# Optimization experiments

Hardware: AMD Instinct MI355X
Metric: run time of the kernel (lower is better)

The kernel has to match this reference:

```python
import jax, jax.numpy as jnp
import numpy as np

N = 100000   # nodes
E = 1600000  # edges per relation
R = 6        # relations
D_IN = 128
H = 64
K = 3


def setup_inputs() -> dict:
    key = jax.random.key(0)
    ks = jax.random.split(key, 20)
    def g(k, shape, scale=0.05):
        return jax.random.normal(k, shape, dtype=jnp.float32) * scale
    return {
        "x": jax.random.normal(ks[0], (N, D_IN), dtype=jnp.float32),
        "edge_index": jax.random.randint(ks[1], (R, 2, E), 0, N, dtype=jnp.int32),
        "cheb1_w": g(ks[2], (R, K, D_IN, H)),
        "cheb1_b": g(ks[3], (R, H)),
        "cheb2_w": g(ks[4], (R, K, H, H)),
        "cheb2_b": g(ks[5], (R, H)),
        "gate_w1": g(ks[6], (H, H)),
        "gate_b1": g(ks[7], (H,)),
        "gate_w2": g(ks[8], (H, 1)),
        "gate_b2": g(ks[9], (1,)),
        "proj_w": g(ks[10], (H, H)),
        "proj_b": g(ks[11], (H,)),
        "cls_w1": g(ks[12], (H, H)),
        "cls_b1": g(ks[13], (H,)),
        "cls_w2": g(ks[14], (H, 1)),
        "cls_b2": g(ks[15], (1,)),
        "aux_w": g(ks[16], (R, H)),
        "aux_b": g(ks[17], (R,)),
    }


def cheb_conv(x, src, dst, W, b, n):
    """PyG ChebConv, sym normalization, lambda_max=2 => L_hat = -D^{-1/2} A D^{-1/2}.
    W: [K, in, out]. Messages flow src -> dst (scatter-add at dst)."""
    deg = jax.ops.segment_sum(jnp.ones(src.shape, x.dtype), src, num_segments=n)
    dis = jnp.where(deg > 0, 1.0 / jnp.sqrt(jnp.maximum(deg, 1e-12)), 0.0)
    norm = -(dis[src] * dis[dst])  # [E]
    def lhat(v):  # sparse SpMM: [N, F] -> [N, F]
        return jax.ops.segment_sum(norm[:, None] * v[src], dst, num_segments=n)
    tx0 = x
    out = tx0 @ W[0]
    tx1 = lhat(x)
    out = out + tx1 @ W[1]
    for k in range(2, W.shape[0]):
        tx2 = 2.0 * lhat(tx1) - tx0
        out = out + tx2 @ W[k]
        tx0, tx1 = tx1, tx2
    return out + b


def reference(x, edge_index, cheb1_w, cheb1_b, cheb2_w, cheb2_b,
              gate_w1, gate_b1, gate_w2, gate_b2, proj_w, proj_b,
              cls_w1, cls_b1, cls_w2, cls_b2, aux_w, aux_b):
    n = x.shape[0]
    hs = []
    for r in range(edge_index.shape[0]):  # small fixed relation set
        src, dst = edge_index[r, 0], edge_index[r, 1]
        h = jax.nn.relu(cheb_conv(x, src, dst, cheb1_w[r], cheb1_b[r], n))
        h = jax.nn.relu(cheb_conv(h, src, dst, cheb2_w[r], cheb2_b[r], n))
        hs.append(h)
    stack = jnp.stack(hs, axis=1)  # [N, R, H]
    # RelationGate: per-(node, relation) MLP -> softmax over relations
    gate_logits = jax.nn.relu(stack @ gate_w1 + gate_b1) @ gate_w2 + gate_b2  # [N, R, 1]
    alpha = jax.nn.softmax(gate_logits, axis=1)
    h_fused = jnp.sum(alpha * stack, axis=1)  # [N, H]
    h_proj = jax.nn.relu(h_fused @ proj_w + proj_b)
    logit = (jax.nn.relu(h_proj @ cls_w1 + cls_b1) @ cls_w2 + cls_b2)[:, 0]  # [N]
    aux = jnp.einsum('nrh,rh->nr', stack, aux_w) + aux_b  # [N, R] aux logits per relation
    return logit, aux
```

## Files before the change

### kernel.cpp

```cpp
#include <hip/hip_runtime.h>
#include <hip/hip_bf16.h>

#define NN 100000
#define EE 1600000
#define RR 6
#define NBK 391
#define EB 391
#define CAP 4608

typedef __attribute__((ext_vector_type(8))) short bf16x8;
typedef __attribute__((ext_vector_type(4))) float f32x4;

__device__ inline short f2b(float x) {
    __hip_bfloat16 h = __float2bfloat16(x);
    return *reinterpret_cast<short*>(&h);
}
__device__ inline float b2f(short s) {
    __hip_bfloat16 h = *reinterpret_cast<__hip_bfloat16*>(&s);
    return __bfloat162float(h);
}


__global__ __launch_bounds__(256) void zero_cnts(int* p, int n) {
    int i = blockIdx.x * 256 + threadIdx.x;
    if (i < n) p[i] = 0;
}

__global__ __launch_bounds__(256) void bin_scatter(const int* __restrict__ src,
                                                   const int* __restrict__ dst,
                                                   int* __restrict__ bcurD,
                                                   int* __restrict__ bcurS,
                                                   unsigned* __restrict__ pairs,
                                                   unsigned char* __restrict__ srcs) {
    __shared__ int lcD[NBK], lbD[NBK], loD[NBK];
    __shared__ int lcS[NBK], lbS[NBK], loS[NBK];
    int t = threadIdx.x;
    for (int i = t; i < NBK; i += 256) { lcD[i] = 0; loD[i] = 0; lcS[i] = 0; loS[i] = 0; }
    __syncthreads();
    int base = blockIdx.x * 4096;
#pragma unroll
    for (int i = 0; i < 16; ++i) {
        int e = base + i * 256 + t;
        if (e < EE) {
            atomicAdd(&lcD[dst[e] >> 8], 1);
            atomicAdd(&lcS[src[e] >> 8], 1);
        }
    }
    __syncthreads();
    for (int i = t; i < NBK; i += 256) {
        lbD[i] = lcD[i] ? atomicAdd(&bcurD[i], lcD[i]) : 0;
        lbS[i] = lcS[i] ? atomicAdd(&bcurS[i], lcS[i]) : 0;
    }
    __syncthreads();
#pragma unroll
    for (int i = 0; i < 16; ++i) {
        int e = base + i * 256 + t;
        if (e < EE) {
            int s = src[e], d = dst[e];
            int bD = d >> 8, bS = s >> 8;
            int pD = lbD[bD] + atomicAdd(&loD[bD], 1);
            if (pD >= 0 && pD < CAP)
                pairs[(size_t)bD * CAP + pD] = ((unsigned)s << 8) | (unsigned)(d & 255);
            int pS = lbS[bS] + atomicAdd(&loS[bS], 1);
            if (pS >= 0 && pS < CAP)
                srcs[(size_t)bS * CAP + pS] = (unsigned char)(s & 255);
        }
    }
}

__global__ __launch_bounds__(512) void csr_build(const unsigned* __restrict__ pairs,
                                                 const int* __restrict__ bcurD,
                                                 int* __restrict__ rowp2,
                                                 int* __restrict__ csr) {
    __shared__ int hist[2048];
    __shared__ int wsums[4];
    int b = blockIdx.x, t = threadIdx.x;
    int p0 = b * CAP;
    int cnt = min(bcurD[b], CAP);
    int p1 = p0 + cnt;
    for (int i = t; i < 2048; i += 512) hist[i] = 0;
    __syncthreads();
    for (int e = p0 + t; e < p1; e += 512) {
        unsigned pr = pairs[e];
        int key = ((pr & 255) << 3) | (int)((pr >> 8) >> 14);
        atomicAdd(&hist[key], 1);
    }
    __syncthreads();
    int s[8] = {0, 0, 0, 0, 0, 0, 0, 0};
    int run = 0, x = 0;
    int lane = t & 63, wv = t >> 6;
    if (t < 256) {
#pragma unroll
        for (int i = 0; i < 8; ++i) { s[i] = run; run += hist[t * 8 + i]; }
        x = run;
#pragma unroll
        for (int d = 1; d < 64; d <<= 1) {
            int y = __shfl_up(x, d, 64);
            if (lane >= d) x += y;
        }
        if (lane == 63) wsums[wv] = x;
    }
    __syncthreads();
    if (t < 256) {
        int woff = 0;
        for (int wi = 0; wi < wv; ++wi) woff += wsums[wi];
        int excl = woff + x - run;
        rowp2[b * 257 + t] = p0 + excl;
        if (t == 0) rowp2[b * 257 + 256] = p1;
#pragma unroll
        for (int i = 0; i < 8; ++i) hist[t * 8 + i] = p0 + excl + s[i];
    }
    __syncthreads();
    for (int e = p0 + t; e < p1; e += 512) {
        unsigned pr = pairs[e];
        int key = ((pr & 255) << 3) | (int)((pr >> 8) >> 14);
        int pos = atomicAdd(&hist[key], 1);
        if (pos >= 0 && pos < NBK * CAP) csr[pos] = (int)(pr >> 8);
    }
}

__global__ __launch_bounds__(256) void deg_dis(const unsigned char* __restrict__ srcs,
                                               const int* __restrict__ bcurS,
                                               float* __restrict__ dis) {
    __shared__ int hist[256];
    int b = blockIdx.x, t = threadIdx.x;
    hist[t] = 0;
    __syncthreads();
    int cnt = min(bcurS[b], CAP);
    const unsigned char* sp = srcs + (size_t)b * CAP;
    for (int e = t; e < cnt; e += 256)
        atomicAdd(&hist[sp[e]], 1);
    __syncthreads();
    int node = b * 256 + t;
    if (node < NN) {
        int d = hist[t];
        dis[node] = d > 0 ? rsqrtf((float)d) : 0.f;
    }
}

__global__ __launch_bounds__(256) void cvt_x(const float* __restrict__ x, short* __restrict__ xb) {
    int i = blockIdx.x * 256 + threadIdx.x;
    if (i >= NN * 128 / 8) return;
    const float* p = x + (size_t)i * 8;
    float4 u0 = *(const float4*)p;
    float4 u1 = *(const float4*)(p + 4);
    bf16x8 t;
    t[0] = f2b(u0.x); t[1] = f2b(u0.y); t[2] = f2b(u0.z); t[3] = f2b(u0.w);
    t[4] = f2b(u1.x); t[5] = f2b(u1.y); t[6] = f2b(u1.z); t[7] = f2b(u1.w);
    *(bf16x8*)(xb + (size_t)i * 8) = t;
}

__global__ __launch_bounds__(256) void wpack_cheb(const float* __restrict__ W, int Kin, int KS,
                                                  short* __restrict__ bh, short* __restrict__ bl) {
    int idx = blockIdx.x * 256 + threadIdx.x;
    int l = idx & 63;
    int q = idx >> 6;
    int s = q % KS; q /= KS;
    int t = q % 12; q /= 12;
    int r = q;
    if (r >= RR) return;
#pragma unroll
    for (int j = 0; j < 8; ++j) {
        int k = s * 32 + ((l >> 4) * 8) + j;
        int n = t * 16 + (l & 15);
        int g = n >> 6, jj = n & 63;
        float v = W[(((size_t)r * 3 + (g == 0 ? 0 : g)) * Kin + k) * 64 + jj];
        if (g == 0) v -= W[(((size_t)r * 3 + 2) * Kin + k) * 64 + jj];
        short hi = f2b(v);
        short lo = f2b(v - b2f(hi));
        bh[(size_t)idx * 8 + j] = hi;
        bl[(size_t)idx * 8 + j] = lo;
    }
}

__global__ __launch_bounds__(256) void wpack64(const float* __restrict__ W,
                                               short* __restrict__ bh, short* __restrict__ bl) {
    int idx = blockIdx.x * 256 + threadIdx.x;
    if (idx >= 512) return;
    int l = idx & 63;
    int s = (idx >> 6) & 1;
    int t = idx >> 7;
#pragma unroll
    for (int j = 0; j < 8; ++j) {
        int k = s * 32 + ((l >> 4) * 8) + j;
        int n = t * 16 + (l & 15);
        float v = W[k * 64 + n];
        short hi = f2b(v);
        short lo = f2b(v - b2f(hi));
        bh[(size_t)idx * 8 + j] = hi;
        bl[(size_t)idx * 8 + j] = lo;
    }
}

template <int KDIM>
__global__ __launch_bounds__(256) void gemm_mfma(const short* __restrict__ A, int lda,
                                                 const short* __restrict__ bph,
                                                 const short* __restrict__ bplo,
                                                 int nt0, int ntn, int s1, int s2,
                                                 short* __restrict__ o0, int ld0,
                                                 short* __restrict__ o1, int ld1,
                                                 short* __restrict__ o2, int ld2,
                                                 const float* __restrict__ bias,
                                                 int scale_from,
                                                 const float* __restrict__ rowscale,
                                                 int do_relu) {
    constexpr int KS = KDIM / 32;
    int w = threadIdx.x >> 6, l = threadIdx.x & 63;
    int rows0 = blockIdx.x * 64 + w * 16;
    int arow = rows0 + (l & 15);
    int kbase = (l >> 4) * 8;
    bf16x8 af[KS];
#pragma unroll
    for (int s = 0; s < KS; ++s) {
        bf16x8 t = {0, 0, 0, 0, 0, 0, 0, 0};
        if (arow < NN) t = *(const bf16x8*)(A + (size_t)arow * lda + s * 32 + kbase);
        af[s] = t;
    }
    for (int t = 0; t < ntn; ++t) {
        f32x4 acc = {0.f, 0.f, 0.f, 0.f};
        const short* bp0 = bph + (((size_t)(nt0 + t) * KS) * 64 + l) * 8;
        const short* bl0 = bplo + (((size_t)(nt0 + t) * KS) * 64 + l) * 8;
#pragma unroll
        for (int s = 0; s < KS; ++s) {
            bf16x8 bh = *(const bf16x8*)(bp0 + (size_t)s * 64 * 8);
            bf16x8 bl = *(const bf16x8*)(bl0 + (size_t)s * 64 * 8);
            acc = __builtin_amdgcn_mfma_f32_16x16x32_bf16(af[s], bh, acc, 0, 0, 0);
            acc = __builtin_amdgcn_mfma_f32_16x16x32_bf16(af[s], bl, acc, 0, 0, 0);
        }
        short* o;
        int ldc, tl;
        if (t < s1) { o = o0; ldc = ld0; tl = t; }
        else if (t < s2) { o = o1; ldc = ld1; tl = t - s1; }
        else { o = o2; ldc = ld2; tl = t - s2; }
        int lcol = (tl << 4) + (l & 15);
        bool scl = (rowscale != nullptr) && (t >= scale_from);
#pragma unroll
        for (int r_ = 0; r_ < 4; ++r_) {
            int row = rows0 + (l >> 4) * 4 + r_;
            if (row >= NN) continue;
            float v = acc[r_];
            if (bias) v += bias[lcol];
            if (do_relu) v = fmaxf(v, 0.f);
            if (scl) v *= rowscale[row];
            o[(size_t)row * ldc + lcol] = f2b(v);
        }
    }
}

template <int MID>
__global__ __launch_bounds__(256) void spmm_bf(const short* __restrict__ v,
                                               const short* __restrict__ aux,
                                               short* __restrict__ outb, int ldc,
                                               const int* __restrict__ csr,
                                               const int* __restrict__ rowp2,
                                               const float* __restrict__ dis,
                                               const float* __restrict__ bias) {
    int t = threadIdx.x;
    int wv = t >> 6, l = t & 63;
    int g = l >> 4, fl = l & 15;
    int row = blockIdx.x * 16 + wv * 4 + g;
    int b = row >> 8, ri = row & 255;
    int s0 = rowp2[b * 257 + ri];
    int s1 = rowp2[b * 257 + ri + 1];
    s0 = max(s0, b * CAP);
    s1 = min(s1, b * CAP + CAP);
    float a0 = 0.f, a1 = 0.f, a2 = 0.f, a3 = 0.f;
    int e = s0;
    int idx[8], nidx[8];
    bool have = (e + 8 <= s1);
    if (have) {
#pragma unroll
        for (int i = 0; i < 8; ++i) idx[i] = csr[e + i];
    }
    while (have) {
        uint2 u[8];
#pragma unroll
        for (int i = 0; i < 8; ++i)
            u[i] = *(const uint2*)(v + (size_t)idx[i] * 64 + fl * 4);
        int en = e + 8;
        bool nhave = (en + 8 <= s1);
        if (nhave) {
#pragma unroll
            for (int i = 0; i < 8; ++i) nidx[i] = csr[en + i];
        }
#pragma unroll
        for (int i = 0; i < 8; ++i) {
            a0 += __uint_as_float(u[i].x << 16);
            a1 += __uint_as_float(u[i].x & 0xffff0000u);
            a2 += __uint_as_float(u[i].y << 16);
            a3 += __uint_as_float(u[i].y & 0xffff0000u);
        }
#pragma unroll
        for (int i = 0; i < 8; ++i) idx[i] = nidx[i];
        e = en;
        have = nhave;
    }
    for (; e < s1; ++e) {
        uint2 u = *(const uint2*)(v + (size_t)csr[e] * 64 + fl * 4);
        a0 += __uint_as_float(u.x << 16);
        a1 += __uint_as_float(u.x & 0xffff0000u);
        a2 += __uint_as_float(u.y << 16);
        a3 += __uint_as_float(u.y & 0xffff0000u);
    }
    float d = dis[row];
    uint2 au = *(const uint2*)(aux + (size_t)row * 64 + fl * 4);
    float v0, v1, v2, v3;
    if (MID) {
        float mm = -2.f * d * d;
        v0 = __uint_as_float(au.x << 16) + mm * a0;
        v1 = __uint_as_float(au.x & 0xffff0000u) + mm * a1;
        v2 = __uint_as_float(au.y << 16) + mm * a2;
        v3 = __uint_as_float(au.y & 0xffff0000u) + mm * a3;
    } else {
        float4 bs = *(const float4*)(bias + fl * 4);
        v0 = fmaxf(__uint_as_float(au.x << 16) - d * a0 + bs.x, 0.f);
        v1 = fmaxf(__uint_as_float(au.x & 0xffff0000u) - d * a1 + bs.y, 0.f);
        v2 = fmaxf(__uint_as_float(au.y << 16) - d * a2 + bs.z, 0.f);
        v3 = fmaxf(__uint_as_float(au.y & 0xffff0000u) - d * a3 + bs.w, 0.f);
    }
    uint2 o;
    o.x = (unsigned)(unsigned short)f2b(v0) | ((unsigned)(unsigned short)f2b(v1) << 16);
    o.y = (unsigned)(unsigned short)f2b(v2) | ((unsigned)(unsigned short)f2b(v3) << 16);
    *(uint2*)(outb + (size_t)row * ldc + fl * 4) = o;
}

__global__ __launch_bounds__(256) void gate_mfma(const short* __restrict__ stack,
                                                 const short* __restrict__ g1h,
                                                 const short* __restrict__ g1l,
                                                 const float* __restrict__ gb1,
                                                 const float* __restrict__ gw2,
                                                 const float* __restrict__ gb2,
                                                 const float* __restrict__ auxw,
                                                 const float* __restrict__ auxb,
                                                 float* __restrict__ glogit,
                                                 float* __restrict__ out) {
    int w = threadIdx.x >> 6, l = threadIdx.x & 63;
    int rows0 = blockIdx.x * 64 + w * 16;
    int arow = rows0 + (l & 15);
    int kbase = (l >> 4) * 8;
    bf16x8 af[2];
#pragma unroll
    for (int s = 0; s < 2; ++s)
        af[s] = *(const bf16x8*)(stack + (size_t)arow * 64 + s * 32 + kbase);
    int rmod = arow % RR;
    float paux = 0.f;
#pragma unroll
    for (int s = 0; s < 2; ++s) {
        const float* aw = auxw + rmod * 64 + s * 32 + kbase;
#pragma unroll
        for (int j = 0; j < 8; ++j) paux = fmaf(b2f(af[s][j]), aw[j], paux);
    }
    paux += __shfl_xor(paux, 16, 64);
    paux += __shfl_xor(paux, 32, 64);
    if (l < 16) out[NN + (size_t)rows0 + l] = paux + auxb[rmod];
    float p[4] = {0.f, 0.f, 0.f, 0.f};
#pragma unroll
    for (int t = 0; t < 4; ++t) {
        f32x4 acc = {0.f, 0.f, 0.f, 0.f};
#pragma unroll
        for (int s = 0; s < 2; ++s) {
            bf16x8 bh = *(const bf16x8*)(g1h + (((size_t)t * 2 + s) * 64 + l) * 8);
            bf16x8 bl = *(const bf16x8*)(g1l + (((size_t)t * 2 + s) * 64 + l) * 8);
            acc = __builtin_amdgcn_mfma_f32_16x16x32_bf16(af[s], bh, acc, 0, 0, 0);
            acc = __builtin_amdgcn_mfma_f32_16x16x32_bf16(af[s], bl, acc, 0, 0, 0);
        }
        int col = t * 16 + (l & 15);
        float b = gb1[col], w2 = gw2[col];
#pragma unroll
        for (int r_ = 0; r_ < 4; ++r_) {
            float h = fmaxf(acc[r_] + b, 0.f);
            p[r_] = fmaf(h, w2, p[r_]);
        }
    }
#pragma unroll
    for (int d = 1; d < 16; d <<= 1) {
#pragma unroll
        for (int r_ = 0; r_ < 4; ++r_) p[r_] += __shfl_xor(p[r_], d, 64);
    }
    if ((l & 15) == 0) {
        float g2 = gb2[0];
#pragma unroll
        for (int r_ = 0; r_ < 4; ++r_) glogit[rows0 + (l >> 4) * 4 + r_] = p[r_] + g2;
    }
}

__global__ __launch_bounds__(256) void fuse_kernel(const short* __restrict__ stack,
                                                   const float* __restrict__ glogit,
                                                   short* __restrict__ hfused) {
    int tid = threadIdx.x;
    int w = tid >> 6, lane = tid & 63;
    int n = blockIdx.x * 4 + w;
    if (n >= NN) return;
    float gl[RR];
    float m = -1e30f;
#pragma unroll
    for (int r = 0; r < RR; r++) {
        gl[r] = glogit[(size_t)n * RR + r];
        m = fmaxf(m, gl[r]);
    }
    float ssum = 0.f;
#pragma unroll
    for (int r = 0; r < RR; r++) {
        gl[r] = __expf(gl[r] - m);
        ssum += gl[r];
    }
    float inv = 1.f / ssum;
    float hf = 0.f;
#pragma unroll
    for (int r = 0; r < RR; r++) {
        float s = b2f(stack[((size_t)n * RR + r) * 64 + lane]);
        hf = fmaf(gl[r] * inv, s, hf);
    }
    hfused[(size_t)n * 64 + lane] = f2b(hf);
}

__global__ __launch_bounds__(256) void cls_mfma(const short* __restrict__ hproj,
                                                const short* __restrict__ c1h,
                                                const short* __restrict__ c1l,
                                                const float* __restrict__ cb1,
                                                const float* __restrict__ cw2,
                                                const float* __restrict__ cb2,
                                                float* __restrict__ out) {
    int w = threadIdx.x >> 6, l = threadIdx.x & 63;
    int rows0 = blockIdx.x * 64 + w * 16;
    int arow = rows0 + (l & 15);
    int kbase = (l >> 4) * 8;
    bf16x8 af[2];
#pragma unroll
    for (int s = 0; s < 2; ++s) {
        bf16x8 t = {0, 0, 0, 0, 0, 0, 0, 0};
        if (arow < NN) t = *(const bf16x8*)(hproj + (size_t)arow * 64 + s * 32 + kbase);
        af[s] = t;
    }
    float p[4] = {0.f, 0.f, 0.f, 0.f};
#pragma unroll
    for (int t = 0; t < 4; ++t) {
        f32x4 acc = {0.f, 0.f, 0.f, 0.f};
#pragma unroll
        for (int s = 0; s < 2; ++s) {
            bf16x8 bh = *(const bf16x8*)(c1h + (((size_t)t * 2 + s) * 64 + l) * 8);
            bf16x8 bl = *(const bf16x8*)(c1l + (((size_t)t * 2 + s) * 64 + l) * 8);
            acc = __builtin_amdgcn_mfma_f32_16x16x32_bf16(af[s], bh, acc, 0, 0, 0);
            acc = __builtin_amdgcn_mfma_f32_16x16x32_bf16(af[s], bl, acc, 0, 0, 0);
        }
        int col = t * 16 + (l & 15);
        float b = cb1[col], w2 = cw2[col];
#pragma unroll
        for (int r_ = 0; r_ < 4; ++r_) {
            float h = fmaxf(acc[r_] + b, 0.f);
            p[r_] = fmaf(h, w2, p[r_]);
        }
    }
#pragma unroll
    for (int d = 1; d < 16; d <<= 1) {
#pragma unroll
        for (int r_ = 0; r_ < 4; ++r_) p[r_] += __shfl_xor(p[r_], d, 64);
    }
    if ((l & 15) == 0) {
        float c2 = cb2[0];
#pragma unroll
        for (int r_ = 0; r_ < 4; ++r_) {
            int row = rows0 + (l >> 4) * 4 + r_;
            if (row < NN) out[row] = p[r_] + c2;
        }
    }
}


extern "C" void kernel_launch(void* const* d_in, const int* in_sizes, int n_in,
                              void* d_out, int out_size, void* d_ws, size_t ws_size,
                              hipStream_t stream) {
    const float* x = (const float*)d_in[0];
    const int* ei = (const int*)d_in[1];
    const float* c1w = (const float*)d_in[2];
    const float* c1b = (const float*)d_in[3];
    const float* c2w = (const float*)d_in[4];
    const float* c2b = (const float*)d_in[5];
    const float* gw1 = (const float*)d_in[6];
    const float* gb1 = (const float*)d_in[7];
    const float* gw2 = (const float*)d_in[8];
    const float* gb2 = (const float*)d_in[9];
    const float* pw = (const float*)d_in[10];
    const float* pb = (const float*)d_in[11];
    const float* cw1 = (const float*)d_in[12];
    const float* cb1 = (const float*)d_in[13];
    const float* cw2 = (const float*)d_in[14];
    const float* cb2 = (const float*)d_in[15];
    const float* auxw = (const float*)d_in[16];
    const float* auxb = (const float*)d_in[17];
    float* out = (float*)d_out;

    char* wsp = (char*)d_ws;
    size_t off = 0;
    auto carve = [&](size_t bytes) -> char* {
        char* p = wsp + off;
        off += (bytes + 255) & ~(size_t)255;
        return p;
    };
    short* stack = (short*)carve((size_t)NN * RR * 64 * 2);
    short* y1b = (short*)carve((size_t)NN * 64 * 2);
    short* y2b = (short*)carve((size_t)NN * 64 * 2);
    short* wb = (short*)carve((size_t)NN * 64 * 2);
    short* h1 = (short*)carve((size_t)NN * 64 * 2);
    short* t0b = (short*)carve((size_t)NN * 64 * 2);
    short* xb = (short*)carve((size_t)NN * 128 * 2);
    float* dis = (float*)carve((size_t)NN * 4);
    int* rowp2 = (int*)carve((size_t)NBK * 257 * 4);
    int* csr = (int*)carve((size_t)NBK * CAP * 4);
    int* cnts = (int*)carve((size_t)2 * RR * NBK * 4);
    short* bp1h = (short*)carve((size_t)RR * 12 * 4 * 64 * 8 * 2);
    short* bp1l = (short*)carve((size_t)RR * 12 * 4 * 64 * 8 * 2);
    short* bp2h = (short*)carve((size_t)RR * 12 * 2 * 64 * 8 * 2);
    short* bp2l = (short*)carve((size_t)RR * 12 * 2 * 64 * 8 * 2);
    short* g1h = (short*)carve((size_t)512 * 8 * 2);
    short* g1l = (short*)carve((size_t)512 * 8 * 2);
    short* pwh = (short*)carve((size_t)512 * 8 * 2);
    short* pwl = (short*)carve((size_t)512 * 8 * 2);
    short* c1h = (short*)carve((size_t)512 * 8 * 2);
    short* c1l = (short*)carve((size_t)512 * 8 * 2);
    float* glogit = (float*)carve((size_t)NN * RR * 4);
    unsigned* pairs = (unsigned*)y1b;
    unsigned char* srcs = (unsigned char*)y2b;
    short* hfused = h1;
    short* hproj = y2b;
    (void)in_sizes; (void)n_in; (void)out_size;

    if (off > ws_size) return;

    zero_cnts<<<(2 * RR * NBK + 255) / 256, 256, 0, stream>>>(cnts, 2 * RR * NBK);
    cvt_x<<<(NN * 128 / 8 + 255) / 256, 256, 0, stream>>>(x, xb);
    wpack_cheb<<<72, 256, 0, stream>>>(c1w, 128, 4, bp1h, bp1l);
    wpack_cheb<<<36, 256, 0, stream>>>(c2w, 64, 2, bp2h, bp2l);
    wpack64<<<2, 256, 0, stream>>>(gw1, g1h, g1l);
    wpack64<<<2, 256, 0, stream>>>(pw, pwh, pwl);
    wpack64<<<2, 256, 0, stream>>>(cw1, c1h, c1l);

    const int GB = 1563;
    for (int r = 0; r < RR; ++r) {
        const int* src = ei + (size_t)r * 2 * EE;
        const int* dst = src + EE;
        const short* b1h = bp1h + (size_t)r * 12 * 4 * 64 * 8;
        const short* b1l = bp1l + (size_t)r * 12 * 4 * 64 * 8;
        const short* b2h = bp2h + (size_t)r * 12 * 2 * 64 * 8;
        const short* b2l = bp2l + (size_t)r * 12 * 2 * 64 * 8;
        int* bcurD = cnts + (size_t)(2 * r + 0) * NBK;
        int* bcurS = cnts + (size_t)(2 * r + 1) * NBK;

        bin_scatter<<<EB, 256, 0, stream>>>(src, dst, bcurD, bcurS, pairs, srcs);
        csr_build<<<NBK, 512, 0, stream>>>(pairs, bcurD, rowp2, csr);
        deg_dis<<<NBK, 256, 0, stream>>>(srcs, bcurS, dis);

        gemm_mfma<128><<<GB, 256, 0, stream>>>(xb, 128, b1h, b1l, 0, 12, 4, 8,
                                               t0b, 64, y1b, 64, y2b, 64,
                                               nullptr, 4, dis, 0);
        spmm_bf<1><<<NN / 16, 256, 0, stream>>>(y2b, y1b, wb, 64, csr, rowp2, dis, nullptr);
        spmm_bf<0><<<NN / 16, 256, 0, stream>>>(wb, t0b, h1, 64, csr, rowp2, dis,
                                                c1b + r * 64);
        gemm_mfma<64><<<GB, 256, 0, stream>>>(h1, 64, b2h, b2l, 0, 12, 4, 8,
                                              t0b, 64, y1b, 64, y2b, 64,
                                              nullptr, 4, dis, 0);
        spmm_bf<1><<<NN / 16, 256, 0, stream>>>(y2b, y1b, wb, 64, csr, rowp2, dis, nullptr);
        spmm_bf<0><<<NN / 16, 256, 0, stream>>>(wb, t0b, stack + r * 64, RR * 64,
                                                csr, rowp2, dis, c2b + r * 64);
    }
    gate_mfma<<<9375, 256, 0, stream>>>(stack, g1h, g1l, gb1, gw2, gb2,
                                        auxw, auxb, glogit, out);
    fuse_kernel<<<NN / 4, 256, 0, stream>>>(stack, glogit, hfused);
    gemm_mfma<64><<<GB, 256, 0, stream>>>(hfused, 64, pwh, pwl, 0, 4, 4, 8,
                                          hproj, 64, nullptr, 0, nullptr, 0,
                                          pb, 99, nullptr, 1);
    cls_mfma<<<GB, 256, 0, stream>>>(hproj, c1h, c1l, cb1, cw2, cb2, out);
}
```

Before: 1.711 ms.

## Widen SpMM loads, fuse gate with softmax fusion, enlarge binning blocks

Result: no change. 1.725 ms (+0.8%).

```diff
diff --git a/kernel.cpp b/kernel.cpp
--- a/kernel.cpp
+++ b/kernel.cpp
@@ -5,7 +5,7 @@
 #define EE 1600000
 #define RR 6
 #define NBK 391
-#define EB 391
+#define EB2 196
 #define CAP 4608
 
 typedef __attribute__((ext_vector_type(8))) short bf16x8;
@@ -18,6 +18,11 @@
 __device__ inline float b2f(short s) {
     __hip_bfloat16 h = *reinterpret_cast<__hip_bfloat16*>(&s);
     return __bfloat162float(h);
+}
+__device__ inline float ulo(unsigned u) { return __uint_as_float(u << 16); }
+__device__ inline float uhi(unsigned u) { return __uint_as_float(u & 0xffff0000u); }
+__device__ inline unsigned pck(float a, float b) {
+    return (unsigned)(unsigned short)f2b(a) | ((unsigned)(unsigned short)f2b(b) << 16);
 }
 
 
@@ -37,9 +42,9 @@
     int t = threadIdx.x;
     for (int i = t; i < NBK; i += 256) { lcD[i] = 0; loD[i] = 0; lcS[i] = 0; loS[i] = 0; }
     __syncthreads();
-    int base = blockIdx.x * 4096;
-#pragma unroll
-    for (int i = 0; i < 16; ++i) {
+    int base = blockIdx.x * 8192;
+#pragma unroll
+    for (int i = 0; i < 32; ++i) {
         int e = base + i * 256 + t;
         if (e < EE) {
             atomicAdd(&lcD[dst[e] >> 8], 1);
@@ -53,7 +58,7 @@
     }
     __syncthreads();
 #pragma unroll
-    for (int i = 0; i < 16; ++i) {
+    for (int i = 0; i < 32; ++i) {
         int e = base + i * 256 + t;
         if (e < EE) {
             int s = src[e], d = dst[e];
@@ -257,14 +262,15 @@
                                                const float* __restrict__ bias) {
     int t = threadIdx.x;
     int wv = t >> 6, l = t & 63;
-    int g = l >> 4, fl = l & 15;
-    int row = blockIdx.x * 16 + wv * 4 + g;
+    int g = l >> 3, fl = l & 7;
+    int row = blockIdx.x * 32 + wv * 8 + g;
+    if (row >= NN) return;
     int b = row >> 8, ri = row & 255;
     int s0 = rowp2[b * 257 + ri];
     int s1 = rowp2[b * 257 + ri + 1];
     s0 = max(s0, b * CAP);
     s1 = min(s1, b * CAP + CAP);
-    float a0 = 0.f, a1 = 0.f, a2 = 0.f, a3 = 0.f;
+    float a[8] = {0.f, 0.f, 0.f, 0.f, 0.f, 0.f, 0.f, 0.f};
     int e = s0;
     int idx[8], nidx[8];
     bool have = (e + 8 <= s1);
@@ -273,10 +279,10 @@
         for (int i = 0; i < 8; ++i) idx[i] = csr[e + i];
     }
     while (have) {
-        uint2 u[8];
+        uint4 u[8];
 #pragma unroll
         for (int i = 0; i < 8; ++i)
-            u[i] = *(const uint2*)(v + (size_t)idx[i] * 64 + fl * 4);
+            u[i] = *(const uint4*)(v + (size_t)idx[i] * 64 + fl * 8);
         int en = e + 8;
         bool nhave = (en + 8 <= s1);
         if (nhave) {
@@ -285,10 +291,10 @@
         }
 #pragma unroll
         for (int i = 0; i < 8; ++i) {
-            a0 += __uint_as_float(u[i].x << 16);
-            a1 += __uint_as_float(u[i].x & 0xffff0000u);
-            a2 += __uint_as_float(u[i].y << 16);
-            a3 += __uint_as_float(u[i].y & 0xffff0000u);
+            a[0] += ulo(u[i].x); a[1] += uhi(u[i].x);
+            a[2] += ulo(u[i].y); a[3] += uhi(u[i].y);
+            a[4] += ulo(u[i].z); a[5] += uhi(u[i].z);
+            a[6] += ulo(u[i].w); a[7] += uhi(u[i].w);
         }
 #pragma unroll
         for (int i = 0; i < 8; ++i) idx[i] = nidx[i];
@@ -296,35 +302,35 @@
         have = nhave;
     }
     for (; e < s1; ++e) {
-        uint2 u = *(const uint2*)(v + (size_t)csr[e] * 64 + fl * 4);
-        a0 += __uint_as_float(u.x << 16);
-        a1 += __uint_as_float(u.x & 0xffff0000u);
-        a2 += __uint_as_float(u.y << 16);
-        a3 += __uint_as_float(u.y & 0xffff0000u);
+        uint4 u = *(const uint4*)(v + (size_t)csr[e] * 64 + fl * 8);
+        a[0] += ulo(u.x); a[1] += uhi(u.x);
+        a[2] += ulo(u.y); a[3] += uhi(u.y);
+        a[4] += ulo(u.z); a[5] += uhi(u.z);
+        a[6] += ulo(u.w); a[7] += uhi(u.w);
     }
     float d = dis[row];
-    uint2 au = *(const uint2*)(aux + (size_t)row * 64 + fl * 4);
-    float v0, v1, v2, v3;
+    uint4 au = *(const uint4*)(aux + (size_t)row * 64 + fl * 8);
+    float av[8] = {ulo(au.x), uhi(au.x), ulo(au.y), uhi(au.y),
+                   ulo(au.z), uhi(au.z), ulo(au.w), uhi(au.w)};
+    float vv[8];
     if (MID) {
         float mm = -2.f * d * d;
-        v0 = __uint_as_float(au.x << 16) + mm * a0;
-        v1 = __uint_as_float(au.x & 0xffff0000u) + mm * a1;
-        v2 = __uint_as_float(au.y << 16) + mm * a2;
-        v3 = __uint_as_float(au.y & 0xffff0000u) + mm * a3;
+#pragma unroll
+        for (int i = 0; i < 8; ++i) vv[i] = av[i] + mm * a[i];
     } else {
-        float4 bs = *(const float4*)(bias + fl * 4);
-        v0 = fmaxf(__uint_as_float(au.x << 16) - d * a0 + bs.x, 0.f);
-        v1 = fmaxf(__uint_as_float(au.x & 0xffff0000u) - d * a1 + bs.y, 0.f);
-        v2 = fmaxf(__uint_as_float(au.y << 16) - d * a2 + bs.z, 0.f);
-        v3 = fmaxf(__uint_as_float(au.y & 0xffff0000u) - d * a3 + bs.w, 0.f);
-    }
-    uint2 o;
-    o.x = (unsigned)(unsigned short)f2b(v0) | ((unsigned)(unsigned short)f2b(v1) << 16);
-    o.y = (unsigned)(unsigned short)f2b(v2) | ((unsigned)(unsigned short)f2b(v3) << 16);
-    *(uint2*)(outb + (size_t)row * ldc + fl * 4) = o;
-}
-
-__global__ __launch_bounds__(256) void gate_mfma(const short* __restrict__ stack,
+        float4 bs0 = *(const float4*)(bias + fl * 8);
+        float4 bs1 = *(const float4*)(bias + fl * 8 + 4);
+        float bb[8] = {bs0.x, bs0.y, bs0.z, bs0.w, bs1.x, bs1.y, bs1.z, bs1.w};
+#pragma unroll
+        for (int i = 0; i < 8; ++i) vv[i] = fmaxf(av[i] - d * a[i] + bb[i], 0.f);
+    }
+    uint4 o;
+    o.x = pck(vv[0], vv[1]); o.y = pck(vv[2], vv[3]);
+    o.z = pck(vv[4], vv[5]); o.w = pck(vv[6], vv[7]);
+    *(uint4*)(outb + (size_t)row * ldc + fl * 8) = o;
+}
+
+__global__ __launch_bounds__(384) void gate_fuse(const short* __restrict__ stack,
                                                  const short* __restrict__ g1h,
                                                  const short* __restrict__ g1l,
                                                  const float* __restrict__ gb1,
@@ -332,86 +338,112 @@
                                                  const float* __restrict__ gb2,
                                                  const float* __restrict__ auxw,
                                                  const float* __restrict__ auxb,
-                                                 float* __restrict__ glogit,
+                                                 short* __restrict__ hfused,
                                                  float* __restrict__ out) {
-    int w = threadIdx.x >> 6, l = threadIdx.x & 63;
-    int rows0 = blockIdx.x * 64 + w * 16;
-    int arow = rows0 + (l & 15);
+    __shared__ float glog[384];
+    __shared__ float alpha[64][6];
+    int t = threadIdx.x;
+    int w = t / 64, l = t & 63;
+    int nb = blockIdx.x * 64;
+    int rowsw = nb * 6 + w * 64;
     int kbase = (l >> 4) * 8;
-    bf16x8 af[2];
-#pragma unroll
-    for (int s = 0; s < 2; ++s)
-        af[s] = *(const bf16x8*)(stack + (size_t)arow * 64 + s * 32 + kbase);
-    int rmod = arow % RR;
-    float paux = 0.f;
-#pragma unroll
-    for (int s = 0; s < 2; ++s) {
-        const float* aw = auxw + rmod * 64 + s * 32 + kbase;
-#pragma unroll
-        for (int j = 0; j < 8; ++j) paux = fmaf(b2f(af[s][j]), aw[j], paux);
-    }
-    paux += __shfl_xor(paux, 16, 64);
-    paux += __shfl_xor(paux, 32, 64);
-    if (l < 16) out[NN + (size_t)rows0 + l] = paux + auxb[rmod];
-    float p[4] = {0.f, 0.f, 0.f, 0.f};
-#pragma unroll
-    for (int t = 0; t < 4; ++t) {
-        f32x4 acc = {0.f, 0.f, 0.f, 0.f};
+    bf16x8 af[4][2];
+#pragma unroll
+    for (int q = 0; q < 4; ++q) {
+        int arow = rowsw + q * 16 + (l & 15);
+        bool ok = arow < NN * RR;
 #pragma unroll
         for (int s = 0; s < 2; ++s) {
-            bf16x8 bh = *(const bf16x8*)(g1h + (((size_t)t * 2 + s) * 64 + l) * 8);
-            bf16x8 bl = *(const bf16x8*)(g1l + (((size_t)t * 2 + s) * 64 + l) * 8);
-            acc = __builtin_amdgcn_mfma_f32_16x16x32_bf16(af[s], bh, acc, 0, 0, 0);
-            acc = __builtin_amdgcn_mfma_f32_16x16x32_bf16(af[s], bl, acc, 0, 0, 0);
-        }
-        int col = t * 16 + (l & 15);
-        float b = gb1[col], w2 = gw2[col];
-#pragma unroll
-        for (int r_ = 0; r_ < 4; ++r_) {
-            float h = fmaxf(acc[r_] + b, 0.f);
-            p[r_] = fmaf(h, w2, p[r_]);
-        }
-    }
-#pragma unroll
-    for (int d = 1; d < 16; d <<= 1) {
-#pragma unroll
-        for (int r_ = 0; r_ < 4; ++r_) p[r_] += __shfl_xor(p[r_], d, 64);
-    }
-    if ((l & 15) == 0) {
-        float g2 = gb2[0];
-#pragma unroll
-        for (int r_ = 0; r_ < 4; ++r_) glogit[rows0 + (l >> 4) * 4 + r_] = p[r_] + g2;
-    }
-}
-
-__global__ __launch_bounds__(256) void fuse_kernel(const short* __restrict__ stack,
-                                                   const float* __restrict__ glogit,
-                                                   short* __restrict__ hfused) {
-    int tid = threadIdx.x;
-    int w = tid >> 6, lane = tid & 63;
-    int n = blockIdx.x * 4 + w;
-    if (n >= NN) return;
-    float gl[RR];
-    float m = -1e30f;
-#pragma unroll
-    for (int r = 0; r < RR; r++) {
-        gl[r] = glogit[(size_t)n * RR + r];
-        m = fmaxf(m, gl[r]);
-    }
-    float ssum = 0.f;
-#pragma unroll
-    for (int r = 0; r < RR; r++) {
-        gl[r] = __expf(gl[r] - m);
-        ssum += gl[r];
-    }
-    float inv = 1.f / ssum;
-    float hf = 0.f;
-#pragma unroll
-    for (int r = 0; r < RR; r++) {
-        float s = b2f(stack[((size_t)n * RR + r) * 64 + lane]);
-        hf = fmaf(gl[r] * inv, s, hf);
-    }
-    hfused[(size_t)n * 64 + lane] = f2b(hf);
+            bf16x8 z = {0, 0, 0, 0, 0, 0, 0, 0};
+            af[q][s] = ok ? *(const bf16x8*)(stack + (size_t)arow * 64 + s * 32 + kbase) : z;
+        }
+        int rmod = arow % RR;
+        float paux = 0.f;
+#pragma unroll
+        for (int s = 0; s < 2; ++s) {
+            const float* aw = auxw + rmod * 64 + s * 32 + kbase;
+#pragma unroll
+            for (int j = 0; j < 8; ++j) paux = fmaf(b2f(af[q][s][j]), aw[j], paux);
+        }
+        paux += __shfl_xor(paux, 16, 64);
+        paux += __shfl_xor(paux, 32, 64);
+        int orow = rowsw + q * 16 + l;
+        if (l < 16 && orow < NN * RR) out[NN + (size_t)orow] = paux + auxb[orow % RR];
+    }
+    float pt[4][4];
+#pragma unroll
+    for (int q = 0; q < 4; ++q)
+#pragma unroll
+        for (int r_ = 0; r_ < 4; ++r_) pt[q][r_] = 0.f;
+#pragma unroll
+    for (int tc = 0; tc < 4; ++tc) {
+        int col = tc * 16 + (l & 15);
+        float bcol = gb1[col], w2 = gw2[col];
+        bf16x8 bh0 = *(const bf16x8*)(g1h + (((size_t)tc * 2 + 0) * 64 + l) * 8);
+        bf16x8 bl0 = *(const bf16x8*)(g1l + (((size_t)tc * 2 + 0) * 64 + l) * 8);
+        bf16x8 bh1 = *(const bf16x8*)(g1h + (((size_t)tc * 2 + 1) * 64 + l) * 8);
+        bf16x8 bl1 = *(const bf16x8*)(g1l + (((size_t)tc * 2 + 1) * 64 + l) * 8);
+#pragma unroll
+        for (int q = 0; q < 4; ++q) {
+            f32x4 acc = {0.f, 0.f, 0.f, 0.f};
+            acc = __builtin_amdgcn_mfma_f32_16x16x32_bf16(af[q][0], bh0, acc, 0, 0, 0);
+            acc = __builtin_amdgcn_mfma_f32_16x16x32_bf16(af[q][0], bl0, acc, 0, 0, 0);
+            acc = __builtin_amdgcn_mfma_f32_16x16x32_bf16(af[q][1], bh1, acc, 0, 0, 0);
+            acc = __builtin_amdgcn_mfma_f32_16x16x32_bf16(af[q][1], bl1, acc, 0, 0, 0);
+#pragma unroll
+            for (int r_ = 0; r_ < 4; ++r_) {
+                float h = fmaxf(acc[r_] + bcol, 0.f);
+                pt[q][r_] = fmaf(h, w2, pt[q][r_]);
+            }
+        }
+    }
+#pragma unroll
+    for (int q = 0; q < 4; ++q) {
+#pragma unroll
+        for (int d = 1; d < 16; d <<= 1)
+#pragma unroll
+            for (int r_ = 0; r_ < 4; ++r_) pt[q][r_] += __shfl_xor(pt[q][r_], d, 64);
+        if ((l & 15) == 0) {
+            float g2 = gb2[0];
+#pragma unroll
+            for (int r_ = 0; r_ < 4; ++r_)
+                glog[w * 64 + q * 16 + (l >> 4) * 4 + r_] = pt[q][r_] + g2;
+        }
+    }
+    __syncthreads();
+    if (t < 64 && nb + t < NN) {
+        float gl[RR];
+        float m = -1e30f;
+#pragma unroll
+        for (int r = 0; r < RR; ++r) {
+            gl[r] = glog[t * 6 + r];
+            m = fmaxf(m, gl[r]);
+        }
+        float ssum = 0.f;
+#pragma unroll
+        for (int r = 0; r < RR; ++r) {
+            gl[r] = __expf(gl[r] - m);
+            ssum += gl[r];
+        }
+        float inv = 1.f / ssum;
+#pragma unroll
+        for (int r = 0; r < RR; ++r) alpha[t][r] = gl[r] * inv;
+    }
+    __syncthreads();
+    for (int i = t; i < 2048; i += 384) {
+        int nl = i >> 5, c2 = (i & 31) * 2;
+        int n = nb + nl;
+        if (n >= NN) break;
+        float hf0 = 0.f, hf1 = 0.f;
+#pragma unroll
+        for (int r = 0; r < RR; ++r) {
+            unsigned u = *(const unsigned*)(stack + ((size_t)n * RR + r) * 64 + c2);
+            float al = alpha[nl][r];
+            hf0 = fmaf(al, ulo(u), hf0);
+            hf1 = fmaf(al, uhi(u), hf1);
+        }
+        *(unsigned*)(hfused + (size_t)n * 64 + c2) = pck(hf0, hf1);
+    }
 }
 
 __global__ __launch_bounds__(256) void cls_mfma(const short* __restrict__ hproj,
@@ -518,7 +550,6 @@
     short* pwl = (short*)carve((size_t)512 * 8 * 2);
     short* c1h = (short*)carve((size_t)512 * 8 * 2);
     short* c1l = (short*)carve((size_t)512 * 8 * 2);
-    float* glogit = (float*)carve((size_t)NN * RR * 4);
     unsigned* pairs = (unsigned*)y1b;
     unsigned char* srcs = (unsigned char*)y2b;
     short* hfused = h1;
@@ -546,26 +577,25 @@
         int* bcurD = cnts + (size_t)(2 * r + 0) * NBK;
         int* bcurS = cnts + (size_t)(2 * r + 1) * NBK;
 
-        bin_scatter<<<EB, 256, 0, stream>>>(src, dst, bcurD, bcurS, pairs, srcs);
+        bin_scatter<<<EB2, 256, 0, stream>>>(src, dst, bcurD, bcurS, pairs, srcs);
         csr_build<<<NBK, 512, 0, stream>>>(pairs, bcurD, rowp2, csr);
         deg_dis<<<NBK, 256, 0, stream>>>(srcs, bcurS, dis);
 
         gemm_mfma<128><<<GB, 256, 0, stream>>>(xb, 128, b1h, b1l, 0, 12, 4, 8,
                                                t0b, 64, y1b, 64, y2b, 64,
                                                nullptr, 4, dis, 0);
-        spmm_bf<1><<<NN / 16, 256, 0, stream>>>(y2b, y1b, wb, 64, csr, rowp2, dis, nullptr);
-        spmm_bf<0><<<NN / 16, 256, 0, stream>>>(wb, t0b, h1, 64, csr, rowp2, dis,
+        spmm_bf<1><<<NN / 32, 256, 0, stream>>>(y2b, y1b, wb, 64, csr, rowp2, dis, nullptr);
+        spmm_bf<0><<<NN / 32, 256, 0, stream>>>(wb, t0b, h1, 64, csr, rowp2, dis,
                                                 c1b + r * 64);
         gemm_mfma<64><<<GB, 256, 0, stream>>>(h1, 64, b2h, b2l, 0, 12, 4, 8,
                                               t0b, 64, y1b, 64, y2b, 64,
                                               nullptr, 4, dis, 0);
-        spmm_bf<1><<<NN / 16, 256, 0, stream>>>(y2b, y1b, wb, 64, csr, rowp2, dis, nullptr);
-        spmm_bf<0><<<NN / 16, 256, 0, stream>>>(wb, t0b, stack + r * 64, RR * 64,
+        spmm_bf<1><<<NN / 32, 256, 0, stream>>>(y2b, y1b, wb, 64, csr, rowp2, dis, nullptr);
+        spmm_bf<0><<<NN / 32, 256, 0, stream>>>(wb, t0b, stack + r * 64, RR * 64,
                                                 csr, rowp2, dis, c2b + r * 64);
     }
-    gate_mfma<<<9375, 256, 0, stream>>>(stack, g1h, g1l, gb1, gw2, gb2,
-                                        auxw, auxb, glogit, out);
-    fuse_kernel<<<NN / 4, 256, 0, stream>>>(stack, glogit, hfused);
+    gate_fuse<<<GB, 384, 0, stream>>>(stack, g1h, g1l, gb1, gw2, gb2,
+                                      auxw, auxb, hfused, out);
     gemm_mfma<64><<<GB, 256, 0, stream>>>(hfused, 64, pwh, pwl, 0, 4, 4, 8,
                                           hproj, 64, nullptr, 0, nullptr, 0,
                                           pb, 99, nullptr, 1);
```
